# Kernel tuning notes

Hardware: AMD Instinct MI355X
Metric: run time of the kernel (lower is better)

Reference implementation:

```python
import jax, jax.numpy as jnp
import numpy as np

N, A, C, S = 65536, 1024, 1000, 2  # S = max aug multiplier from self.augs


def _update_cv(x, labels, cov_prior, ave_prior, amount_prior):
    # Efficient segment-reduce form of update_CV (original builds O(N*C*A) onehot tensor)
    cnt = jax.ops.segment_sum(jnp.ones((N,), x.dtype), labels, num_segments=C)  # [C]
    sum_c = jax.ops.segment_sum(x, labels, num_segments=C)                      # [C,A]
    cnt_c = jnp.where(cnt == 0, 1.0, cnt)                                       # Amount_CxA clamp
    ave = sum_c / cnt_c[:, None]                                                # ave_CxA
    var = jax.ops.segment_sum((x - ave[labels]) ** 2, labels, num_segments=C) / cnt_c[:, None]
    var = jnp.where(var == 0, 1e-10, var)
    w = (cnt / (cnt + amount_prior + 1e-10))[:, None]                           # weight_CV [C,1]
    additional = w * (1 - w) * (ave_prior - ave) ** 2
    new_cov = cov_prior * (1 - w) + var * w + additional
    new_ave = ave_prior * (1 - w) + ave * w
    new_amount = amount_prior + cnt
    return new_cov, new_ave, new_amount


def setup_inputs() -> dict:
    key = jax.random.key(0)
    ks = jax.random.split(key, 6)
    return {
        "x": jax.random.normal(ks[0], (N, A), jnp.float32),
        "eps": jax.random.normal(ks[1], (S, C, A), jnp.float32),
        "fc_w": jax.random.normal(ks[2], (C, A), jnp.float32) * 0.02,
        "fc_b": jnp.zeros((C,), jnp.float32),
        "ba_coeffi": jax.random.normal(ks[3], (C,), jnp.float32) * 0.1,
        "cov_prior": jax.random.uniform(ks[4], (C, A), jnp.float32) * 0.01,
        "ave_prior": jnp.zeros((C, A), jnp.float32),
        "amount_prior": jnp.zeros((C,), jnp.float32),
        "target_x": jax.random.randint(ks[5], (N,), 0, C).astype(jnp.int64),
    }


def reference(x, eps, fc_w, fc_b, ba_coeffi, cov_prior, ave_prior, amount_prior, target_x):
    # update_CV runs under torch.no_grad -> stop_gradient on stats
    new_cov, new_ave, _ = _update_cv(x, target_x, cov_prior, ave_prior, amount_prior)
    new_cov = jax.lax.stop_gradient(new_cov)
    new_ave = jax.lax.stop_gradient(new_ave)
    # Gaussian augmentation: Normal(loc=Ave, scale=CoVariance).sample((S,)) per class
    aug = new_ave[None, :, :] + new_cov[None, :, :] * eps  # [S,C,A]
    aug = aug.reshape(S * C, A)
    aug_labels = jnp.tile(jnp.arange(C, dtype=target_x.dtype), S)
    feats = jnp.concatenate([x, aug], axis=0)              # [N+S*C, A]
    labels_all = jnp.concatenate([target_x, aug_labels], axis=0)
    logits = feats @ fc_w.T + fc_b - ba_coeffi             # [N+S*C, C]
    logp = jax.nn.log_softmax(logits, axis=-1)
    loss = -jnp.mean(jnp.take_along_axis(logp, labels_all[:, None], axis=1))
    return loss
```

## Files before the change

### kernel.cpp

```cpp
#include <hip/hip_runtime.h>

#define NROWS 65536
#define ADIM  1024
#define CCLS  1000
#define SAUG  2
#define MROWS (NROWS + SAUG*CCLS)
#define MPAD  67584
#define NPAD  1024
#define NPART 4
#define NEG_INF (-3.0e38f)

typedef __bf16 bf16x8 __attribute__((ext_vector_type(8)));
typedef float  f32x4  __attribute__((ext_vector_type(4)));
typedef unsigned short u16;

__device__ __forceinline__ unsigned pk2bf(float a, float b){
  unsigned ua = __float_as_uint(a), ub = __float_as_uint(b);
  ua = (ua + 0x7FFFu + ((ua>>16)&1u)) >> 16;
  ub = (ub + 0x7FFFu + ((ub>>16)&1u)) >> 16;
  return ua | (ub<<16);
}
__device__ __forceinline__ float bflo(unsigned u){ return __uint_as_float((u & 0xFFFFu) << 16); }
__device__ __forceinline__ float bfhi(unsigned u){ return __uint_as_float(u & 0xFFFF0000u); }

__global__ void k_hist(const int* __restrict__ tgt, int* __restrict__ cnt){
  int i = blockIdx.x*blockDim.x + threadIdx.x;
  int stride = gridDim.x*blockDim.x;
  for (; i < NROWS; i += stride) atomicAdd(&cnt[tgt[i]], 1);
}

__global__ void k_scan(const int* __restrict__ cnt, int* __restrict__ start){
  __shared__ int s[1024];
  int t = threadIdx.x;
  int v = (t < CCLS) ? cnt[t] : 0;
  s[t] = v;
  __syncthreads();
  for (int off = 1; off < 1024; off <<= 1){
    int u = (t >= off) ? s[t-off] : 0;
    __syncthreads();
    s[t] += u;
    __syncthreads();
  }
  if (t < CCLS) start[t] = s[t] - v;
}

__global__ void k_scatter(const int* __restrict__ tgt, const int* __restrict__ start,
                          int* __restrict__ pos, int* __restrict__ sorted){
  int i = blockIdx.x*blockDim.x + threadIdx.x;
  int stride = gridDim.x*blockDim.x;
  for (; i < NROWS; i += stride){
    int c = tgt[i];
    int r = atomicAdd(&pos[c], 1);
    sorted[start[c] + r] = i;
  }
}

__global__ void k_cvt_x(const float* __restrict__ x, u16* __restrict__ xb){
  size_t i = ((size_t)blockIdx.x*blockDim.x + threadIdx.x)*8;
  float4 a = *(const float4*)(x+i);
  float4 b = *(const float4*)(x+i+4);
  uint4 o;
  o.x = pk2bf(a.x,a.y); o.y = pk2bf(a.z,a.w);
  o.z = pk2bf(b.x,b.y); o.w = pk2bf(b.z,b.w);
  *(uint4*)(xb+i) = o;
}

__global__ void k_pad(u16* __restrict__ xb){
  size_t i = ((size_t)blockIdx.x*blockDim.x + threadIdx.x)*8 + (size_t)MROWS*ADIM;
  uint4 z = {0u,0u,0u,0u};
  *(uint4*)(xb+i) = z;
}

__global__ void k_cvt_w(const float* __restrict__ w, u16* __restrict__ wb){
  size_t i = ((size_t)blockIdx.x*blockDim.x + threadIdx.x)*8;
  int row = (int)(i >> 10);
  uint4 o = {0u,0u,0u,0u};
  if (row < CCLS){
    float4 a = *(const float4*)(w+i);
    float4 b = *(const float4*)(w+i+4);
    o.x = pk2bf(a.x,a.y); o.y = pk2bf(a.z,a.w);
    o.z = pk2bf(b.x,b.y); o.w = pk2bf(b.z,b.w);
  }
  *(uint4*)(wb+i) = o;
}

__global__ void k_bias(const float* __restrict__ fc_b, const float* __restrict__ ba,
                       float* __restrict__ biasv){
  int c = blockIdx.x*blockDim.x + threadIdx.x;
  if (c < NPAD) biasv[c] = (c < CCLS) ? fc_b[c] - ba[c] : NEG_INF;
}

__global__ void k_stats(const u16* __restrict__ xb_in, const int* __restrict__ sorted,
                        const int* __restrict__ cnt, const int* __restrict__ start,
                        const float* __restrict__ amt_p, const float* __restrict__ cov_p,
                        const float* __restrict__ ave_p, const float* __restrict__ eps,
                        u16* __restrict__ xb){
  int c = blockIdx.x;
  int t = threadIdx.x;
  int col = t*4;
  int n = cnt[c];
  int st = start[c];
  float s[4] = {0.f,0.f,0.f,0.f}, q[4] = {0.f,0.f,0.f,0.f};
  for (int i = 0; i < n; i++){
    int row = sorted[st + i];
    const uint2 uv = *(const uint2*)(xb_in + (size_t)row*ADIM + col);
    float v0 = bflo(uv.x), v1 = bfhi(uv.x), v2 = bflo(uv.y), v3 = bfhi(uv.y);
    s[0]+=v0; s[1]+=v1; s[2]+=v2; s[3]+=v3;
    q[0]+=v0*v0; q[1]+=v1*v1; q[2]+=v2*v2; q[3]+=v3*v3;
  }
  float cf = (float)n;
  float cc = (n == 0) ? 1.f : cf;
  float wgt = cf / (cf + amt_p[c] + 1e-10f);
  float4 cv = *(const float4*)(cov_p + (size_t)c*ADIM + col);
  float4 av = *(const float4*)(ave_p + (size_t)c*ADIM + col);
  float cvp[4] = {cv.x,cv.y,cv.z,cv.w};
  float avp[4] = {av.x,av.y,av.z,av.w};
  float ncov[4], nave[4];
  #pragma unroll
  for (int j = 0; j < 4; j++){
    float ave = s[j]/cc;
    float var = (q[j] - 2.f*ave*s[j] + cf*ave*ave)/cc;
    if (var <= 0.f) var = 1e-10f;
    float add = wgt*(1.f-wgt)*(avp[j]-ave)*(avp[j]-ave);
    ncov[j] = cvp[j]*(1.f-wgt) + var*wgt + add;
    nave[j] = avp[j]*(1.f-wgt) + ave*wgt;
  }
  #pragma unroll
  for (int s_ = 0; s_ < SAUG; s_++){
    size_t eoff = ((size_t)(s_*CCLS + c))*ADIM + col;
    size_t roff = ((size_t)(NROWS + s_*CCLS + c))*ADIM + col;
    const float4 e = *(const float4*)(eps + eoff);
    uint2 o;
    o.x = pk2bf(nave[0]+ncov[0]*e.x, nave[1]+ncov[1]*e.y);
    o.y = pk2bf(nave[2]+ncov[2]*e.z, nave[3]+ncov[3]*e.w);
    *(uint2*)(xb + roff) = o;
  }
}

__global__ __launch_bounds__(512,2) void k_gemm_part(
    const u16* __restrict__ xb, const u16* __restrict__ wb,
    const float* __restrict__ biasv, const int* __restrict__ tgt,
    float* __restrict__ pm, float* __restrict__ pl, float* __restrict__ plab){
  extern __shared__ char smem[];
  const int t = threadIdx.x;
  const int lane = t & 63;
  const int wv = t >> 6;
  const int wr = wv >> 2;
  const int wc = wv & 3;
  const int col = lane & 15;
  const int quad = lane >> 4;

  const int bid = blockIdx.x;
  const int wg  = (bid & 7)*132 + (bid >> 3);
  const int sp  = wg & 3;
  const int row0 = (wg >> 2) * 256;

  const unsigned lds0 = (unsigned)(size_t)((__attribute__((address_space(3))) char*)smem);

  unsigned aoff[8], boff[4];
  #pragma unroll
  for (int m = 0; m < 8; m++){
    unsigned lin = (unsigned)((wr*128 + m*16 + col)*64 + quad*16);
    aoff[m] = lds0 + (lin ^ (((lin >> 7) & 3u) << 4));
  }
  #pragma unroll
  for (int n = 0; n < 4; n++){
    unsigned lin = (unsigned)((wc*64 + n*16 + col)*64 + quad*16);
    boff[n] = lds0 + 16384u + (lin ^ (((lin >> 7) & 3u) << 4));
  }

  const u16* src[4];
  int dstoff[4];
  {
    const u16* gA = xb + (size_t)row0*ADIM;
    const u16* gB = wb + (size_t)(sp*256)*ADIM;
    #pragma unroll
    for (int j = 0; j < 4; j++){
      unsigned d = (unsigned)((j & 1)*8192 + wv*1024 + lane*16);
      unsigned s = d ^ ((((unsigned)lane >> 3) & 3u) << 4);
      src[j] = (j < 2 ? gA : gB) + (size_t)(s >> 6)*ADIM + ((s & 63u) >> 1);
      dstoff[j] = (j < 2 ? 0 : 16384) + (j & 1)*8192 + wv*1024;
    }
  }

#define STG(tile, nb, j) \
  __builtin_amdgcn_global_load_lds( \
      (const __attribute__((address_space(1))) void*)(src[j] + (size_t)(tile)*32), \
      (__attribute__((address_space(3))) void*)(smem + (nb)*32768 + dstoff[j]), 16, 0, 0)

  f32x4 acc[8][4];
  const f32x4 z = {0.f,0.f,0.f,0.f};
  #pragma unroll
  for (int m = 0; m < 8; m++)
    #pragma unroll
    for (int n = 0; n < 4; n++) acc[m][n] = z;

  #pragma unroll
  for (int p = 0; p < 3; p++){
    STG(p, p, 0); STG(p, p, 1); STG(p, p, 2); STG(p, p, 3);
  }

  for (int kt = 0; kt < 29; kt++){
    const int cb = kt & 3, nb = (kt + 3) & 3;
    const unsigned cbo = (unsigned)(cb << 15);
    bf16x8 af[4], bfr[4];
    STG(kt+3, nb, 0); STG(kt+3, nb, 1);
    asm volatile("s_waitcnt vmcnt(10)" ::: "memory");
    __builtin_amdgcn_sched_barrier(0);
    __builtin_amdgcn_s_barrier();
    __builtin_amdgcn_sched_barrier(0);
    #pragma unroll
    for (int m = 0; m < 4; m++)
      asm volatile("ds_read_b128 %0, %1" : "=v"(af[m]) : "v"(aoff[m]+cbo));
    #pragma unroll
    for (int n = 0; n < 4; n++)
      asm volatile("ds_read_b128 %0, %1" : "=v"(bfr[n]) : "v"(boff[n]+cbo));
    asm volatile("s_waitcnt lgkmcnt(0)" ::: "memory");
    __builtin_amdgcn_sched_barrier(0);
    __builtin_amdgcn_s_setprio(1);
    #pragma unroll
    for (int m = 0; m < 4; m++)
      #pragma unroll
      for (int n = 0; n < 4; n++)
        acc[m][n] = __builtin_amdgcn_mfma_f32_16x16x32_bf16(af[m], bfr[n], acc[m][n], 0, 0, 0);
    __builtin_amdgcn_s_setprio(0);
    STG(kt+3, nb, 2); STG(kt+3, nb, 3);
    #pragma unroll
    for (int m = 0; m < 4; m++)
      asm volatile("ds_read_b128 %0, %1" : "=v"(af[m]) : "v"(aoff[4+m]+cbo));
    asm volatile("s_waitcnt lgkmcnt(0)" ::: "memory");
    __builtin_amdgcn_sched_barrier(0);
    __builtin_amdgcn_s_setprio(1);
    #pragma unroll
    for (int m = 0; m < 4; m++)
      #pragma unroll
      for (int n = 0; n < 4; n++)
        acc[4+m][n] = __builtin_amdgcn_mfma_f32_16x16x32_bf16(af[m], bfr[n], acc[4+m][n], 0, 0, 0);
    __builtin_amdgcn_s_setprio(0);
    __builtin_amdgcn_sched_barrier(0);
    __builtin_amdgcn_s_barrier();
  }

  asm volatile("s_waitcnt vmcnt(0)" ::: "memory");
  __builtin_amdgcn_sched_barrier(0);
  __builtin_amdgcn_s_barrier();
  #pragma unroll
  for (int kt = 29; kt < 32; kt++){
    const unsigned cbo = (unsigned)((kt & 3) << 15);
    bf16x8 af[4], bfr[4];
    #pragma unroll
    for (int m = 0; m < 4; m++)
      asm volatile("ds_read_b128 %0, %1" : "=v"(af[m]) : "v"(aoff[m]+cbo));
    #pragma unroll
    for (int n = 0; n < 4; n++)
      asm volatile("ds_read_b128 %0, %1" : "=v"(bfr[n]) : "v"(boff[n]+cbo));
    asm volatile("s_waitcnt lgkmcnt(0)" ::: "memory");
    __builtin_amdgcn_sched_barrier(0);
    #pragma unroll
    for (int m = 0; m < 4; m++)
      #pragma unroll
      for (int n = 0; n < 4; n++)
        acc[m][n] = __builtin_amdgcn_mfma_f32_16x16x32_bf16(af[m], bfr[n], acc[m][n], 0, 0, 0);
    #pragma unroll
    for (int m = 0; m < 4; m++)
      asm volatile("ds_read_b128 %0, %1" : "=v"(af[m]) : "v"(aoff[4+m]+cbo));
    asm volatile("s_waitcnt lgkmcnt(0)" ::: "memory");
    __builtin_amdgcn_sched_barrier(0);
    #pragma unroll
    for (int m = 0; m < 4; m++)
      #pragma unroll
      for (int n = 0; n < 4; n++)
        acc[4+m][n] = __builtin_amdgcn_mfma_f32_16x16x32_bf16(af[m], bfr[n], acc[4+m][n], 0, 0, 0);
  }
#undef STG

  float bias[4];
  #pragma unroll
  for (int n = 0; n < 4; n++) bias[n] = biasv[sp*256 + wc*64 + n*16 + col];

  __syncthreads();
  float* red = (float*)smem;

  #pragma unroll
  for (int m = 0; m < 8; m++){
    #pragma unroll
    for (int rg = 0; rg < 4; rg++){
      const int rb = wr*128 + m*16 + quad*4 + rg;
      const int gr = row0 + rb;
      int lbl = -1;
      if (gr < NROWS) lbl = tgt[gr];
      else if (gr < MROWS){ int a_ = gr - NROWS; lbl = (a_ < CCLS) ? a_ : a_ - CCLS; }
      float lg[4];
      float mx = NEG_INF, lv = NEG_INF;
      #pragma unroll
      for (int n = 0; n < 4; n++){
        float v = acc[m][n][rg] + bias[n];
        lg[n] = v;
        mx = fmaxf(mx, v);
        int c = sp*256 + wc*64 + n*16 + col;
        lv = (c == lbl) ? v : lv;
      }
      #pragma unroll
      for (int o = 1; o < 16; o <<= 1) mx = fmaxf(mx, __shfl_xor(mx, o));
      float se = 0.f;
      #pragma unroll
      for (int n = 0; n < 4; n++) se += __expf(lg[n] - mx);
      #pragma unroll
      for (int o = 1; o < 16; o <<= 1) se += __shfl_xor(se, o);
      #pragma unroll
      for (int o = 1; o < 16; o <<= 1) lv = fmaxf(lv, __shfl_xor(lv, o));
      if (col == 0){
        red[0*1024 + rb*4 + wc] = mx;
        red[1*1024 + rb*4 + wc] = se;
        red[2*1024 + rb*4 + wc] = lv;
      }
    }
  }
  __syncthreads();
  if (t < 256){
    float m0 = red[t*4+0], m1 = red[t*4+1], m2 = red[t*4+2], m3 = red[t*4+3];
    float mx = fmaxf(fmaxf(m0,m1), fmaxf(m2,m3));
    float l  = red[1024+t*4+0]*__expf(m0-mx) + red[1024+t*4+1]*__expf(m1-mx)
             + red[1024+t*4+2]*__expf(m2-mx) + red[1024+t*4+3]*__expf(m3-mx);
    float lv = fmaxf(fmaxf(red[2048+t*4+0],red[2048+t*4+1]),
                     fmaxf(red[2048+t*4+2],red[2048+t*4+3]));
    size_t idx = (size_t)sp*MPAD + (size_t)(row0 + t);
    pm[idx]   = mx;
    pl[idx]   = l;
    plab[idx] = lv;
  }
}

__global__ void k_merge(const float* __restrict__ pm, const float* __restrict__ pl,
                        const float* __restrict__ plab, float* __restrict__ out){
  int r = blockIdx.x*256 + threadIdx.x;
  float v = 0.f;
  if (r < MROWS){
    float m = NEG_INF, lb = NEG_INF;
    #pragma unroll
    for (int s = 0; s < NPART; s++){
      m  = fmaxf(m,  pm[(size_t)s*MPAD + r]);
      lb = fmaxf(lb, plab[(size_t)s*MPAD + r]);
    }
    float l = 0.f;
    #pragma unroll
    for (int s = 0; s < NPART; s++)
      l += pl[(size_t)s*MPAD + r]*__expf(pm[(size_t)s*MPAD + r] - m);
    v = (m + __logf(l) - lb) * (1.0f/(float)MROWS);
  }
  #pragma unroll
  for (int o = 32; o > 0; o >>= 1) v += __shfl_xor(v, o);
  if ((threadIdx.x & 63) == 0) atomicAdd(out, v);
}

extern "C" void kernel_launch(void* const* d_in, const int* in_sizes, int n_in,
                              void* d_out, int out_size, void* d_ws, size_t ws_size,
                              hipStream_t stream) {
  const float* x     = (const float*)d_in[0];
  const float* eps   = (const float*)d_in[1];
  const float* fc_w  = (const float*)d_in[2];
  const float* fc_b  = (const float*)d_in[3];
  const float* ba    = (const float*)d_in[4];
  const float* cov_p = (const float*)d_in[5];
  const float* ave_p = (const float*)d_in[6];
  const float* amt_p = (const float*)d_in[7];
  const int*   tgt   = (const int*)d_in[8];
  float* out = (float*)d_out;

  char* ws = (char*)d_ws;
  u16*   xb    = (u16*)(ws);
  u16*   wb    = (u16*)(ws + 138412032u);
  float* biasv = (float*)(ws + 140509184u);
  int*   sorted= (int*)(ws + 140513280u);
  int*   cnt   = (int*)(ws + 140775424u);
  int*   pos   = (int*)(ws + 140779520u);
  int*   start = (int*)(ws + 140783616u);
  float* pm    = (float*)(ws + 140787712u);
  float* pl    = (float*)(ws + 142950400u);
  float* plab  = (float*)(ws + 145113088u);

  static int cfg = 0;
  if (!cfg){
    hipFuncSetAttribute((const void*)k_gemm_part,
                        hipFuncAttributeMaxDynamicSharedMemorySize, 131072);
    cfg = 1;
  }

  hipMemsetAsync(cnt, 0, 12288, stream);
  hipMemsetAsync(out, 0, sizeof(float), stream);

  k_hist   <<<256, 256, 0, stream>>>(tgt, cnt);
  k_scan   <<<1, 1024, 0, stream>>>(cnt, start);
  k_scatter<<<256, 256, 0, stream>>>(tgt, start, pos, sorted);
  k_cvt_x  <<<32768, 256, 0, stream>>>(x, xb);
  k_pad    <<<24, 256, 0, stream>>>(xb);
  k_cvt_w  <<<512, 256, 0, stream>>>(fc_w, wb);
  k_bias   <<<4, 256, 0, stream>>>(fc_b, ba, biasv);
  k_stats  <<<CCLS, 256, 0, stream>>>(xb, sorted, cnt, start, amt_p, cov_p, ave_p, eps, xb);
  k_gemm_part<<<1056, 512, 131072, stream>>>(xb, wb, biasv, tgt, pm, pl, plab);
  k_merge  <<<264, 256, 0, stream>>>(pm, pl, plab, out);
}
```

Before: 705.9 us.

## Software-pipeline LDS fragment reads against MFMA and batch stats-kernel gathers

The GEMM main loop is rewritten so that each iteration issues LDS reads for the next K-tile into a second register set while MFMAs consume the current one. It uses one barrier per tile instead of two, and LDS reads use immediate offsets instead of precomputed per-fragment addresses. The stats kernel stages row indices in shared memory and unrolls the gather by four, so several independent loads are in flight at once. Together these aim to hide LDS and global load latency, at the cost of doubled fragment registers, which may reduce occupancy or cause spills.

```diff
diff --git a/kernel.cpp b/kernel.cpp
--- a/kernel.cpp
+++ b/kernel.cpp
@@ -95,18 +95,53 @@
                         const float* __restrict__ amt_p, const float* __restrict__ cov_p,
                         const float* __restrict__ ave_p, const float* __restrict__ eps,
                         u16* __restrict__ xb){
+  __shared__ int sidx[256];
   int c = blockIdx.x;
   int t = threadIdx.x;
   int col = t*4;
   int n = cnt[c];
   int st = start[c];
   float s[4] = {0.f,0.f,0.f,0.f}, q[4] = {0.f,0.f,0.f,0.f};
-  for (int i = 0; i < n; i++){
-    int row = sorted[st + i];
-    const uint2 uv = *(const uint2*)(xb_in + (size_t)row*ADIM + col);
-    float v0 = bflo(uv.x), v1 = bfhi(uv.x), v2 = bflo(uv.y), v3 = bfhi(uv.y);
-    s[0]+=v0; s[1]+=v1; s[2]+=v2; s[3]+=v3;
-    q[0]+=v0*v0; q[1]+=v1*v1; q[2]+=v2*v2; q[3]+=v3*v3;
+  for (int base = 0; base < n; base += 256){
+    int m = min(256, n - base);
+    __syncthreads();
+    if (t < m) sidx[t] = sorted[st + base + t];
+    __syncthreads();
+    int i = 0;
+    for (; i + 4 <= m; i += 4){
+      int r0 = sidx[i], r1 = sidx[i+1], r2 = sidx[i+2], r3 = sidx[i+3];
+      uint2 u0 = *(const uint2*)(xb_in + (size_t)r0*ADIM + col);
+      uint2 u1 = *(const uint2*)(xb_in + (size_t)r1*ADIM + col);
+      uint2 u2 = *(const uint2*)(xb_in + (size_t)r2*ADIM + col);
+      uint2 u3 = *(const uint2*)(xb_in + (size_t)r3*ADIM + col);
+      {
+        float v0=bflo(u0.x), v1=bfhi(u0.x), v2=bflo(u0.y), v3=bfhi(u0.y);
+        s[0]+=v0; s[1]+=v1; s[2]+=v2; s[3]+=v3;
+        q[0]+=v0*v0; q[1]+=v1*v1; q[2]+=v2*v2; q[3]+=v3*v3;
+      }
+      {
+        float v0=bflo(u1.x), v1=bfhi(u1.x), v2=bflo(u1.y), v3=bfhi(u1.y);
+        s[0]+=v0; s[1]+=v1; s[2]+=v2; s[3]+=v3;
+        q[0]+=v0*v0; q[1]+=v1*v1; q[2]+=v2*v2; q[3]+=v3*v3;
+      }
+      {
+        float v0=bflo(u2.x), v1=bfhi(u2.x), v2=bflo(u2.y), v3=bfhi(u2.y);
+        s[0]+=v0; s[1]+=v1; s[2]+=v2; s[3]+=v3;
+        q[0]+=v0*v0; q[1]+=v1*v1; q[2]+=v2*v2; q[3]+=v3*v3;
+      }
+      {
+        float v0=bflo(u3.x), v1=bfhi(u3.x), v2=bflo(u3.y), v3=bfhi(u3.y);
+        s[0]+=v0; s[1]+=v1; s[2]+=v2; s[3]+=v3;
+        q[0]+=v0*v0; q[1]+=v1*v1; q[2]+=v2*v2; q[3]+=v3*v3;
+      }
+    }
+    for (; i < m; i++){
+      int row = sidx[i];
+      const uint2 uv = *(const uint2*)(xb_in + (size_t)row*ADIM + col);
+      float v0 = bflo(uv.x), v1 = bfhi(uv.x), v2 = bflo(uv.y), v3 = bfhi(uv.y);
+      s[0]+=v0; s[1]+=v1; s[2]+=v2; s[3]+=v3;
+      q[0]+=v0*v0; q[1]+=v1*v1; q[2]+=v2*v2; q[3]+=v3*v3;
+    }
   }
   float cf = (float)n;
   float cc = (n == 0) ? 1.f : cf;
@@ -157,36 +192,71 @@
 
   const unsigned lds0 = (unsigned)(size_t)((__attribute__((address_space(3))) char*)smem);
 
-  unsigned aoff[8], boff[4];
-  #pragma unroll
-  for (int m = 0; m < 8; m++){
-    unsigned lin = (unsigned)((wr*128 + m*16 + col)*64 + quad*16);
-    aoff[m] = lds0 + (lin ^ (((lin >> 7) & 3u) << 4));
-  }
-  #pragma unroll
-  for (int n = 0; n < 4; n++){
-    unsigned lin = (unsigned)((wc*64 + n*16 + col)*64 + quad*16);
-    boff[n] = lds0 + 16384u + (lin ^ (((lin >> 7) & 3u) << 4));
-  }
-
-  const u16* src[4];
-  int dstoff[4];
+  unsigned aB[4], bB[4];
   {
-    const u16* gA = xb + (size_t)row0*ADIM;
-    const u16* gB = wb + (size_t)(sp*256)*ADIM;
+    unsigned linA = (unsigned)((wr*128 + col)*64 + quad*16);
+    unsigned swzA = linA ^ (((linA >> 7) & 3u) << 4);
+    unsigned linB = (unsigned)((wc*64 + col)*64 + quad*16);
+    unsigned swzB = linB ^ (((linB >> 7) & 3u) << 4);
     #pragma unroll
-    for (int j = 0; j < 4; j++){
-      unsigned d = (unsigned)((j & 1)*8192 + wv*1024 + lane*16);
-      unsigned s = d ^ ((((unsigned)lane >> 3) & 3u) << 4);
-      src[j] = (j < 2 ? gA : gB) + (size_t)(s >> 6)*ADIM + ((s & 63u) >> 1);
-      dstoff[j] = (j < 2 ? 0 : 16384) + (j & 1)*8192 + wv*1024;
+    for (int qq = 0; qq < 4; qq++){
+      aB[qq] = lds0 + qq*32768 + swzA;
+      bB[qq] = lds0 + qq*32768 + 16384 + swzB;
     }
   }
 
-#define STG(tile, nb, j) \
-  __builtin_amdgcn_global_load_lds( \
-      (const __attribute__((address_space(1))) void*)(src[j] + (size_t)(tile)*32), \
-      (__attribute__((address_space(3))) void*)(smem + (nb)*32768 + dstoff[j]), 16, 0, 0)
+  const u16* gA = xb + (size_t)row0*ADIM;
+  const u16* gB = wb + (size_t)(sp*256)*ADIM;
+  unsigned off_[2];
+  const int ldsd = wv*1024;
+  #pragma unroll
+  for (int jj = 0; jj < 2; jj++){
+    unsigned d = (unsigned)(jj*8192 + wv*1024 + lane*16);
+    unsigned sv = d ^ (((d >> 7) & 3u) << 4);
+    off_[jj] = (sv >> 6)*ADIM + ((sv & 63u) >> 1);
+  }
+
+#define STG4(TILE, NB) do{ \
+  __builtin_amdgcn_global_load_lds((const __attribute__((address_space(1))) void*)(gA + off_[0] + (TILE)*32), \
+      (__attribute__((address_space(3))) void*)(smem + (NB)*32768 + ldsd), 16, 0, 0); \
+  __builtin_amdgcn_global_load_lds((const __attribute__((address_space(1))) void*)(gA + off_[1] + (TILE)*32), \
+      (__attribute__((address_space(3))) void*)(smem + (NB)*32768 + 8192 + ldsd), 16, 0, 0); \
+  __builtin_amdgcn_global_load_lds((const __attribute__((address_space(1))) void*)(gB + off_[0] + (TILE)*32), \
+      (__attribute__((address_space(3))) void*)(smem + (NB)*32768 + 16384 + ldsd), 16, 0, 0); \
+  __builtin_amdgcn_global_load_lds((const __attribute__((address_space(1))) void*)(gB + off_[1] + (TILE)*32), \
+      (__attribute__((address_space(3))) void*)(smem + (NB)*32768 + 24576 + ldsd), 16, 0, 0); \
+}while(0)
+
+#define DSR(dst, base, off) asm volatile("ds_read_b128 %0, %1 offset:" #off : "=v"(dst) : "v"(base))
+#define READT(QN, NA, NB) do{ \
+  DSR(NA[0], aB[QN], 0);    DSR(NA[1], aB[QN], 1024); DSR(NA[2], aB[QN], 2048); DSR(NA[3], aB[QN], 3072); \
+  DSR(NA[4], aB[QN], 4096); DSR(NA[5], aB[QN], 5120); DSR(NA[6], aB[QN], 6144); DSR(NA[7], aB[QN], 7168); \
+  DSR(NB[0], bB[QN], 0);    DSR(NB[1], bB[QN], 1024); DSR(NB[2], bB[QN], 2048); DSR(NB[3], bB[QN], 3072); \
+}while(0)
+
+#define MFMAT(CA, CB) do{ \
+  _Pragma("unroll") \
+  for (int m_ = 0; m_ < 8; m_++){ \
+    _Pragma("unroll") \
+    for (int n_ = 0; n_ < 4; n_++) \
+      acc[m_][n_] = __builtin_amdgcn_mfma_f32_16x16x32_bf16(CA[m_], CB[n_], acc[m_][n_], 0, 0, 0); \
+  } \
+}while(0)
+
+#define BODY(TILE3, QN, QS, CA, CB, NA, NB) do{ \
+  __builtin_amdgcn_s_barrier(); \
+  __builtin_amdgcn_sched_barrier(0); \
+  STG4((TILE3), QS); \
+  asm volatile("s_waitcnt vmcnt(4)" ::: "memory"); \
+  __builtin_amdgcn_sched_barrier(0); \
+  READT(QN, NA, NB); \
+  asm volatile("s_waitcnt lgkmcnt(12)" ::: "memory"); \
+  __builtin_amdgcn_sched_barrier(0); \
+  __builtin_amdgcn_s_setprio(1); \
+  MFMAT(CA, CB); \
+  __builtin_amdgcn_s_setprio(0); \
+  __builtin_amdgcn_sched_barrier(0); \
+}while(0)
 
   f32x4 acc[8][4];
   const f32x4 z = {0.f,0.f,0.f,0.f};
@@ -195,84 +265,53 @@
     #pragma unroll
     for (int n = 0; n < 4; n++) acc[m][n] = z;
 
-  #pragma unroll
-  for (int p = 0; p < 3; p++){
-    STG(p, p, 0); STG(p, p, 1); STG(p, p, 2); STG(p, p, 3);
-  }
-
-  for (int kt = 0; kt < 29; kt++){
-    const int cb = kt & 3, nb = (kt + 3) & 3;
-    const unsigned cbo = (unsigned)(cb << 15);
-    bf16x8 af[4], bfr[4];
-    STG(kt+3, nb, 0); STG(kt+3, nb, 1);
-    asm volatile("s_waitcnt vmcnt(10)" ::: "memory");
-    __builtin_amdgcn_sched_barrier(0);
-    __builtin_amdgcn_s_barrier();
-    __builtin_amdgcn_sched_barrier(0);
-    #pragma unroll
-    for (int m = 0; m < 4; m++)
-      asm volatile("ds_read_b128 %0, %1" : "=v"(af[m]) : "v"(aoff[m]+cbo));
-    #pragma unroll
-    for (int n = 0; n < 4; n++)
-      asm volatile("ds_read_b128 %0, %1" : "=v"(bfr[n]) : "v"(boff[n]+cbo));
-    asm volatile("s_waitcnt lgkmcnt(0)" ::: "memory");
-    __builtin_amdgcn_sched_barrier(0);
-    __builtin_amdgcn_s_setprio(1);
-    #pragma unroll
-    for (int m = 0; m < 4; m++)
-      #pragma unroll
-      for (int n = 0; n < 4; n++)
-        acc[m][n] = __builtin_amdgcn_mfma_f32_16x16x32_bf16(af[m], bfr[n], acc[m][n], 0, 0, 0);
-    __builtin_amdgcn_s_setprio(0);
-    STG(kt+3, nb, 2); STG(kt+3, nb, 3);
-    #pragma unroll
-    for (int m = 0; m < 4; m++)
-      asm volatile("ds_read_b128 %0, %1" : "=v"(af[m]) : "v"(aoff[4+m]+cbo));
-    asm volatile("s_waitcnt lgkmcnt(0)" ::: "memory");
-    __builtin_amdgcn_sched_barrier(0);
-    __builtin_amdgcn_s_setprio(1);
-    #pragma unroll
-    for (int m = 0; m < 4; m++)
-      #pragma unroll
-      for (int n = 0; n < 4; n++)
-        acc[4+m][n] = __builtin_amdgcn_mfma_f32_16x16x32_bf16(af[m], bfr[n], acc[4+m][n], 0, 0, 0);
-    __builtin_amdgcn_s_setprio(0);
-    __builtin_amdgcn_sched_barrier(0);
-    __builtin_amdgcn_s_barrier();
-  }
-
+  bf16x8 pA[8], pB[4], oA[8], oB[4];
+
+  STG4(0, 0); STG4(1, 1); STG4(2, 2);
+  asm volatile("s_waitcnt vmcnt(4)" ::: "memory");
+  __builtin_amdgcn_sched_barrier(0);
+  __builtin_amdgcn_s_barrier();
+  __builtin_amdgcn_sched_barrier(0);
+  READT(0, pA, pB);
+
+  for (int b4 = 0; b4 < 7; b4++){
+    const int kt = b4*4;
+    BODY(kt+3, 1, 3, pA, pB, oA, oB);
+    BODY(kt+4, 2, 0, oA, oB, pA, pB);
+    BODY(kt+5, 3, 1, pA, pB, oA, oB);
+    BODY(kt+6, 0, 2, oA, oB, pA, pB);
+  }
+
+  BODY(31, 1, 3, pA, pB, oA, oB);
+  __builtin_amdgcn_s_barrier();
+  __builtin_amdgcn_sched_barrier(0);
   asm volatile("s_waitcnt vmcnt(0)" ::: "memory");
   __builtin_amdgcn_sched_barrier(0);
+  READT(2, pA, pB);
+  asm volatile("s_waitcnt lgkmcnt(12)" ::: "memory");
+  __builtin_amdgcn_sched_barrier(0);
+  __builtin_amdgcn_s_setprio(1);
+  MFMAT(oA, oB);
+  __builtin_amdgcn_s_setprio(0);
   __builtin_amdgcn_s_barrier();
-  #pragma unroll
-  for (int kt = 29; kt < 32; kt++){
-    const unsigned cbo = (unsigned)((kt & 3) << 15);
-    bf16x8 af[4], bfr[4];
-    #pragma unroll
-    for (int m = 0; m < 4; m++)
-      asm volatile("ds_read_b128 %0, %1" : "=v"(af[m]) : "v"(aoff[m]+cbo));
-    #pragma unroll
-    for (int n = 0; n < 4; n++)
-      asm volatile("ds_read_b128 %0, %1" : "=v"(bfr[n]) : "v"(boff[n]+cbo));
-    asm volatile("s_waitcnt lgkmcnt(0)" ::: "memory");
-    __builtin_amdgcn_sched_barrier(0);
-    #pragma unroll
-    for (int m = 0; m < 4; m++)
-      #pragma unroll
-      for (int n = 0; n < 4; n++)
-        acc[m][n] = __builtin_amdgcn_mfma_f32_16x16x32_bf16(af[m], bfr[n], acc[m][n], 0, 0, 0);
-    #pragma unroll
-    for (int m = 0; m < 4; m++)
-      asm volatile("ds_read_b128 %0, %1" : "=v"(af[m]) : "v"(aoff[4+m]+cbo));
-    asm volatile("s_waitcnt lgkmcnt(0)" ::: "memory");
-    __builtin_amdgcn_sched_barrier(0);
-    #pragma unroll
-    for (int m = 0; m < 4; m++)
-      #pragma unroll
-      for (int n = 0; n < 4; n++)
-        acc[4+m][n] = __builtin_amdgcn_mfma_f32_16x16x32_bf16(af[m], bfr[n], acc[4+m][n], 0, 0, 0);
-  }
-#undef STG
+  __builtin_amdgcn_sched_barrier(0);
+  READT(3, oA, oB);
+  asm volatile("s_waitcnt lgkmcnt(12)" ::: "memory");
+  __builtin_amdgcn_sched_barrier(0);
+  __builtin_amdgcn_s_setprio(1);
+  MFMAT(pA, pB);
+  __builtin_amdgcn_s_setprio(0);
+  asm volatile("s_waitcnt lgkmcnt(0)" ::: "memory");
+  __builtin_amdgcn_sched_barrier(0);
+  __builtin_amdgcn_s_setprio(1);
+  MFMAT(oA, oB);
+  __builtin_amdgcn_s_setprio(0);
+
+#undef BODY
+#undef MFMAT
+#undef READT
+#undef DSR
+#undef STG4
 
   float bias[4];
   #pragma unroll
```

Result: no change. 719.2 us (+1.9%).
